# Optimization experiments

Hardware: AMD Instinct MI355X
Metric: run time of the kernel (lower is better)

The kernel has to match this reference:

```python
import jax, jax.numpy as jnp
import numpy as np

B, C = 2, 128
FMAP_HW = [(256, 256), (128, 128), (64, 64), (32, 32)]
N_ROIS = 4000
POOL = (7, 7)
N_ANCH = 300000
N_POS = 1000          # anchors with match > 0 (class 1)
N_NEG = 200000        # anchors with match == -1
SHEM_POOLSIZE = 20
N_CLASSES = 2


def setup_inputs() -> dict:
    key = jax.random.key(0)
    ks = jax.random.split(key, 10)
    inp = {}
    for l, (h, w) in enumerate(FMAP_HW):
        inp[f"fmap{l}"] = jax.random.normal(ks[l], (B, C, h, w), dtype=jnp.float32)
    # rois: normalized (y1, x1, y2, x2, batch_ix)
    ctr = jax.random.uniform(ks[4], (N_ROIS, 2))
    sz = jax.random.uniform(ks[5], (N_ROIS, 2), minval=0.02, maxval=0.5)
    lo = jnp.clip(ctr - sz / 2, 0.0, 1.0)
    hi = jnp.clip(ctr + sz / 2, 0.0, 1.0)
    bix = jax.random.randint(ks[6], (N_ROIS, 1), 0, B).astype(jnp.float32)
    inp["rois"] = jnp.concatenate([lo, hi, bix], axis=1)
    # fixed layout for static shapes: [pos | neg | neutral]
    am = np.zeros(N_ANCH, np.int32)
    am[:N_POS] = 1
    am[N_POS:N_POS + N_NEG] = -1
    inp["anchor_matches"] = jnp.asarray(am)
    inp["class_pred_logits"] = jax.random.normal(ks[7], (N_ANCH, N_CLASSES), dtype=jnp.float32)
    inp["pred_deltas"] = jax.random.normal(ks[8], (N_ANCH, 4), dtype=jnp.float32) * 0.1
    inp["target_deltas"] = jax.random.normal(ks[9], (N_ANCH, 4), dtype=jnp.float32) * 0.1
    return inp


def _roi_align_2d(fmap, boxes, batch_ix, pool):
    """Bilinear ROI align, one sample at each bin center.
    fmap: [B,C,H,W]; boxes: [N,4] in fmap pixel coords (y1,x1,y2,x2).
    Returns [N,C,ph,pw]."""
    Hc, Wc = fmap.shape[2], fmap.shape[3]
    ph, pw = pool
    y1, x1, y2, x2 = boxes[:, 0], boxes[:, 1], boxes[:, 2], boxes[:, 3]
    bh = (y2 - y1) / ph
    bw = (x2 - x1) / pw
    iy = jnp.arange(ph, dtype=jnp.float32) + 0.5
    ix = jnp.arange(pw, dtype=jnp.float32) + 0.5
    sy = jnp.clip(y1[:, None] + bh[:, None] * iy[None, :], 0.0, Hc - 1.0)  # [N,ph]
    sx = jnp.clip(x1[:, None] + bw[:, None] * ix[None, :], 0.0, Wc - 1.0)  # [N,pw]
    y0f = jnp.floor(sy)
    x0f = jnp.floor(sx)
    y0 = y0f.astype(jnp.int32)
    x0 = x0f.astype(jnp.int32)
    y1i = jnp.minimum(y0 + 1, Hc - 1)
    x1i = jnp.minimum(x0 + 1, Wc - 1)
    wy = (sy - y0f)[:, :, None, None]  # [N,ph,1,1]
    wx = (sx - x0f)[:, None, :, None]  # [N,1,pw,1]
    b = batch_ix[:, None, None]

    def gather(yy, xx):
        # yy [N,ph], xx [N,pw] -> [N,ph,pw,C]
        return fmap[b, :, yy[:, :, None], xx[:, None, :]]

    v00 = gather(y0, x0)
    v01 = gather(y0, x1i)
    v10 = gather(y1i, x0)
    v11 = gather(y1i, x1i)
    out = (v00 * (1 - wy) * (1 - wx) + v01 * (1 - wy) * wx
           + v10 * wy * (1 - wx) + v11 * wy * wx)
    return jnp.transpose(out, (0, 3, 1, 2))


def _forward(fmaps, rois, anchor_matches, class_pred_logits, pred_deltas, target_deltas):
    boxes = rois[:, :4]
    batch_ix = rois[:, 4].astype(jnp.int32)
    h = boxes[:, 2] - boxes[:, 0]
    w = boxes[:, 3] - boxes[:, 1]
    roi_level = jnp.clip(
        jnp.round(4.0 + jnp.log2(jnp.sqrt(h * w + 1e-12))).astype(jnp.int32), 0, 3)
    boxes_sg = jax.lax.stop_gradient(boxes)  # original detaches level_boxes
    pooled = jnp.zeros((N_ROIS, C, POOL[0], POOL[1]), fmaps[0].dtype)
    for lvl, f in enumerate(fmaps):
        He, We = f.shape[2], f.shape[3]
        lb = boxes_sg * jnp.array([He, We, He, We], jnp.float32)
        pl = _roi_align_2d(f, lb, batch_ix, POOL)
        mask = (roi_level == lvl).astype(pl.dtype)[:, None, None, None]
        pooled = pooled + mask * pl  # each roi hits exactly one level; order preserved

    # ---- class loss with SHEM (layout: [:N_POS] pos, [N_POS:N_POS+N_NEG] neg) ----
    pos_logits = class_pred_logits[:N_POS]
    pos_targets = anchor_matches[:N_POS].astype(jnp.int32)
    pos_logp = jax.nn.log_softmax(pos_logits, axis=1)
    pos_loss = -jnp.mean(jnp.take_along_axis(pos_logp, pos_targets[:, None], axis=1))

    neg_logits = class_pred_logits[N_POS:N_POS + N_NEG]
    neg_bg_prob = jax.nn.softmax(neg_logits, axis=1)[:, 0]
    negative_count = N_POS  # max(1, n_pos)
    pool_n = min(negative_count * SHEM_POOLSIZE, N_NEG)
    order = jnp.argsort(neg_bg_prob)          # ascending bg prob = hardest first
    pool_idx = order[:pool_n]
    perm = jax.random.permutation(jax.random.key(1), pool_n)
    neg_ix = pool_idx[perm[:negative_count]]  # stochastic draw from hard pool
    neg_loss = -jnp.mean(jax.nn.log_softmax(neg_logits[neg_ix], axis=1)[:, 0])
    class_loss = (pos_loss + neg_loss) / 2.0

    # ---- bbox smooth-L1 on positives (beta=1, mean reduction) ----
    diff = jnp.abs(pred_deltas[:N_POS] - target_deltas[:N_POS])
    sl1 = jnp.where(diff < 1.0, 0.5 * diff * diff, diff - 0.5)
    bbox_loss = jnp.mean(sl1)
    return pooled, class_loss, bbox_loss


def reference(fmap0, fmap1, fmap2, fmap3, rois, anchor_matches,
              class_pred_logits, pred_deltas, target_deltas):
    return _forward([fmap0, fmap1, fmap2, fmap3], rois, anchor_matches,
                    class_pred_logits, pred_deltas, target_deltas)
```

## Files before the change

kernel.cpp:

```cpp
#include <hip/hip_runtime.h>
#include <hip/hip_bf16.h>
#include <cstdint>

#define NROIS  4000
#define NCH    128
#define NBINS  49
#define N_POSA 1000
#define N_NEGA 200000
#define POOLN  20000
#define HBITS_A 13
#define ABINS  8192
#define PBINS  4096
#define SUBN   4096
#define NTRBLK 2720
#define NPREP  106
#define NRANKA 512
#define NRANKP 40
#define TPAD   136
#define NSC    145

#define L0OFF 0ull
#define L1OFF 16777216ull
#define L2OFF 20971520ull
#define L3OFF 22020096ull
#define TLELEMS 22282240ull

__device__ __forceinline__ uint32_t rotl32d(uint32_t v, int r) { return (v << r) | (v >> (32-r)); }

__device__ void tf2x32(uint32_t k0, uint32_t k1, uint32_t& x0, uint32_t& x1)
{
    const uint32_t ks2 = k0 ^ k1 ^ 0x1BD11BDAu;
    const int R0[4] = {13,15,26,6};
    const int R1[4] = {17,29,16,24};
    x0 += k0; x1 += k1;
#pragma unroll
    for (int r = 0; r < 4; ++r) { x0 += x1; x1 = rotl32d(x1, R0[r]); x1 ^= x0; }
    x0 += k1;  x1 += ks2 + 1u;
#pragma unroll
    for (int r = 0; r < 4; ++r) { x0 += x1; x1 = rotl32d(x1, R1[r]); x1 ^= x0; }
    x0 += ks2; x1 += k0 + 2u;
#pragma unroll
    for (int r = 0; r < 4; ++r) { x0 += x1; x1 = rotl32d(x1, R0[r]); x1 ^= x0; }
    x0 += k0;  x1 += k1 + 3u;
#pragma unroll
    for (int r = 0; r < 4; ++r) { x0 += x1; x1 = rotl32d(x1, R1[r]); x1 ^= x0; }
    x0 += k1;  x1 += ks2 + 4u;
#pragma unroll
    for (int r = 0; r < 4; ++r) { x0 += x1; x1 = rotl32d(x1, R0[r]); x1 ^= x0; }
    x0 += ks2; x1 += k0 + 5u;
}

__device__ __forceinline__ unsigned int monobits(float x) {
    unsigned int u = __float_as_uint(x);
    return (u & 0x80000000u) ? ~u : (u | 0x80000000u);
}

__device__ __forceinline__ unsigned short f2bf(float x) {
    union { __hip_bfloat16 h; unsigned short u; } c;
    c.h = __float2bfloat16(x);
    return c.u;
}

__global__ void k_zero(unsigned int* __restrict__ h, unsigned int* __restrict__ rA,
                       unsigned int* __restrict__ rP1, unsigned int* __restrict__ rP2)
{
    const int b = blockIdx.x;
    const int i = b*256 + threadIdx.x;
    if      (b <  64) h[i] = 0u;
    else if (b <  96) rA[i - 64*256] = 0u;
    else if (b < 112) rP1[i - 96*256] = 0u;
    else              rP2[i - 112*256] = 0u;
}

__global__ __launch_bounds__(256) void k_trprep(
    const float* __restrict__ f0, const float* __restrict__ f1,
    const float* __restrict__ f2, const float* __restrict__ f3,
    __hip_bfloat16* __restrict__ tl,
    unsigned long long* __restrict__ T1, unsigned long long* __restrict__ T2,
    unsigned int* __restrict__ histA,
    unsigned int* __restrict__ histP1, unsigned int* __restrict__ histP2,
    const int* __restrict__ am, const float* __restrict__ logits,
    const float* __restrict__ pd, const float* __restrict__ td,
    float* __restrict__ prt, int ntr)
{
    __shared__ __align__(16) unsigned char smraw[32768];
    const int bid = blockIdx.x;
    const int t   = threadIdx.x;

    if (bid < ntr) {
        unsigned short* s = (unsigned short*)smraw;
        const int bz = bid / 1360;
        const int r  = bid - bz*1360;
        int lvl, tile;
        if      (r < 1024) { lvl = 0; tile = r; }
        else if (r < 1280) { lvl = 1; tile = r - 1024; }
        else if (r < 1344) { lvl = 2; tile = r - 1280; }
        else               { lvl = 3; tile = r - 1344; }
        const int HW = 65536 >> (2*lvl);
        const float* in = (lvl==0) ? f0 : (lvl==1) ? f1 : (lvl==2) ? f2 : f3;
        const size_t ooff = (lvl==0) ? L0OFF : (lvl==1) ? L1OFF : (lvl==2) ? L2OFF : L3OFF;
        const int hw0 = tile * 64;
        const float4* in4 = (const float4*)(in + (size_t)bz * 128 * HW);
        const int HW4 = HW >> 2;
        const int h4b = hw0 >> 2;
#pragma unroll
        for (int k = 0; k < 8; ++k) {
            const int idx = t + k*256;
            const int c   = idx >> 4;
            const int h4  = idx & 15;
            const float4 v = in4[(size_t)c * HW4 + h4b + h4];
            const int r0 = h4 * 4;
            const int cs = c ^ ((h4 & 7) << 3);
            s[(r0+0)*TPAD + cs] = f2bf(v.x);
            s[(r0+1)*TPAD + cs] = f2bf(v.y);
            s[(r0+2)*TPAD + cs] = f2bf(v.z);
            s[(r0+3)*TPAD + cs] = f2bf(v.w);
        }
        __syncthreads();
        uint4* out4 = (uint4*)(tl + ooff + (size_t)bz * (size_t)HW * 128
                                         + (size_t)hw0 * 128);
        const int rr = t >> 4;
        const int q  = t & 15;
        const int c8 = q * 8;
#pragma unroll
        for (int m = 0; m < 4; ++m) {
            const int row = rr + m*16;
            const int sw = ((row >> 2) & 7) << 3;
            out4[row*16 + q] = *(const uint4*)&s[row*TPAD + (c8 ^ sw)];
        }
        return;
    }

    const int pbid = bid - ntr;
    if (pbid < 40) {
        unsigned int* buf = (unsigned int*)smraw;
        unsigned int* lh1 = buf;
        unsigned int* lh2 = buf + PBINS;
        for (int b = t; b < 2*PBINS; b += 256) buf[b] = 0u;
        __syncthreads();
        const int i = pbid*256 + t;
        if (i < POOLN/2) {
            uint32_t a0 = 0u, a1 = 2u; tf2x32(0u, 1u, a0, a1);
            uint32_t b0 = 1u, b1 = 3u; tf2x32(0u, 1u, b0, b1);
            uint32_t c0 = 0u, c1 = 2u; tf2x32(a0, b0, c0, c1);
            uint32_t d0 = 1u, d1 = 3u; tf2x32(a0, b0, d0, d1);
            uint32_t x0 = (uint32_t)i, x1 = (uint32_t)(POOLN/2 + i);
            tf2x32(a1, b1, x0, x1);
            T1[i]           = ((unsigned long long)x0 << 32) | (unsigned)i;
            T1[POOLN/2 + i] = ((unsigned long long)x1 << 32) | (unsigned)(POOLN/2 + i);
            atomicAdd(&lh1[x0 >> 20], 1u);
            atomicAdd(&lh1[x1 >> 20], 1u);
            uint32_t y0 = (uint32_t)i, y1 = (uint32_t)(POOLN/2 + i);
            tf2x32(c1, d1, y0, y1);
            T2[i]           = ((unsigned long long)y0 << 32) | (unsigned)i;
            T2[POOLN/2 + i] = ((unsigned long long)y1 << 32) | (unsigned)(POOLN/2 + i);
            atomicAdd(&lh2[y0 >> 20], 1u);
            atomicAdd(&lh2[y1 >> 20], 1u);
        }
        __syncthreads();
        for (int b = t; b < PBINS; b += 256) {
            unsigned int v = lh1[b]; if (v) atomicAdd(&histP1[b], v);
            v = lh2[b];              if (v) atomicAdd(&histP2[b], v);
        }
        return;
    }
    if (pbid < 104) {
        unsigned int* buf = (unsigned int*)smraw;
        for (int b = t; b < ABINS; b += 256) buf[b] = 0u;
        __syncthreads();
        for (int i = (pbid-40)*256 + t; i < N_NEGA; i += 64*256) {
            const float l0 = logits[(size_t)(N_POSA+i)*2+0];
            const float l1 = logits[(size_t)(N_POSA+i)*2+1];
            atomicAdd(&buf[monobits(l0 - l1) >> (32-HBITS_A)], 1u);
        }
        __syncthreads();
        for (int b = t; b < ABINS; b += 256) {
            const unsigned int v = buf[b];
            if (v) atomicAdd(&histA[b], v);
        }
        return;
    }
    float* red = (float*)smraw;
    float s = 0.0f;
    if (pbid == 104) {
        for (int i = t; i < N_POSA; i += 256) {
            const int tgt = am[i];
            const float l0 = logits[(size_t)i*2+0], l1 = logits[(size_t)i*2+1];
            const float m = fmaxf(l0, l1);
            const float lse = logf(expf(l0-m) + expf(l1-m));
            const float lt = (tgt == 0) ? l0 : l1;
            s += (lt - m) - lse;
        }
    } else {
        for (int i = t; i < N_POSA*4; i += 256) {
            const float d = fabsf(pd[i] - td[i]);
            s += (d < 1.0f) ? 0.5f*d*d : d - 0.5f;
        }
    }
    red[t] = s;
    __syncthreads();
    for (int off = 128; off > 0; off >>= 1) {
        if (t < off) red[t] += red[t+off];
        __syncthreads();
    }
    if (t == 0) prt[pbid - 104] = red[0];
}

__device__ void scan_one256(const unsigned int* __restrict__ hist,
                            unsigned int* __restrict__ base, int n, unsigned int* lds)
{
    const int t = threadIdx.x;
    const int chunk = n >> 8;
    unsigned int s = 0;
    for (int k = 0; k < chunk; ++k) s += hist[t*chunk + k];
    lds[t] = s;
    __syncthreads();
    for (int off = 1; off < 256; off <<= 1) {
        unsigned int v = (t >= off) ? lds[t-off] : 0u;
        __syncthreads();
        lds[t] += v;
        __syncthreads();
    }
    unsigned int run = (t == 0) ? 0u : lds[t-1];
    for (int k = 0; k < chunk; ++k) {
        base[t*chunk+k] = run;
        run += hist[t*chunk+k];
    }
    if (t == 255) base[n] = run;
    __syncthreads();
}

__device__ void do_roi(int n, const __hip_bfloat16* __restrict__ tl,
                       const float* __restrict__ rois, float* __restrict__ out,
                       unsigned char* smraw)
{
    int   (*s_a)[4] = (int(*)[4])smraw;
    float (*s_w)[4] = (float(*)[4])(smraw + 784);
    float* s_o      = (float*)(smraw + 1568);
    const int tid = threadIdx.x;

    const float ry1 = rois[n*5+0], rx1 = rois[n*5+1];
    const float ry2 = rois[n*5+2], rx2 = rois[n*5+3];
    const int   b   = (int)rois[n*5+4];
    const float h = ry2 - ry1, w = rx2 - rx1;
    const float lraw = rintf(4.0f + log2f(sqrtf(h*w + 1e-12f)));
    int lvl = (int)lraw; lvl = lvl < 0 ? 0 : (lvl > 3 ? 3 : lvl);
    const int H = 256 >> lvl;
    const size_t lbase = (lvl==0) ? L0OFF : (lvl==1) ? L1OFF : (lvl==2) ? L2OFF : L3OFF;
    const __hip_bfloat16* bp = tl + lbase + (size_t)b * (size_t)(H*H) * NCH;

    const float Hf  = (float)H;
    const float y1p = ry1*Hf, x1p = rx1*Hf, y2p = ry2*Hf, x2p = rx2*Hf;
    const float bh = (y2p - y1p) / 7.0f, bw = (x2p - x1p) / 7.0f;

    if (tid < NBINS) {
        const int py = tid / 7, px = tid % 7;
        float sy = y1p + bh*((float)py + 0.5f);
        float sx = x1p + bw*((float)px + 0.5f);
        sy = fminf(fmaxf(sy, 0.0f), Hf - 1.0f);
        sx = fminf(fmaxf(sx, 0.0f), Hf - 1.0f);
        const float y0f = floorf(sy), x0f = floorf(sx);
        const int y0 = (int)y0f, x0 = (int)x0f;
        const int y1i = min(y0+1, H-1), x1i = min(x0+1, H-1);
        const float wy = sy - y0f, wx = sx - x0f;
        s_a[tid][0] = y0 *H + x0;
        s_a[tid][1] = y0 *H + x1i;
        s_a[tid][2] = y1i*H + x0;
        s_a[tid][3] = y1i*H + x1i;
        const float omy = 1.0f - wy, omx = 1.0f - wx;
        s_w[tid][0] = omy*omx; s_w[tid][1] = omy*wx;
        s_w[tid][2] = wy *omx; s_w[tid][3] = wy *wx;
    }
    __syncthreads();

    const int c4 = tid & 31;
    const int bg = tid >> 5;
    for (int bin = bg; bin < NBINS; bin += 8) {
        float a0 = 0.f, a1 = 0.f, a2 = 0.f, a3 = 0.f;
#pragma unroll
        for (int tap = 0; tap < 4; ++tap) {
            const uint2 v = *(const uint2*)(bp + (size_t)s_a[bin][tap] * NCH + 4*c4);
            const float wgt = s_w[bin][tap];
            a0 += __uint_as_float(v.x << 16)         * wgt;
            a1 += __uint_as_float(v.x & 0xffff0000u) * wgt;
            a2 += __uint_as_float(v.y << 16)         * wgt;
            a3 += __uint_as_float(v.y & 0xffff0000u) * wgt;
        }
        s_o[(4*c4+0)*NBINS + bin] = a0;
        s_o[(4*c4+1)*NBINS + bin] = a1;
        s_o[(4*c4+2)*NBINS + bin] = a2;
        s_o[(4*c4+3)*NBINS + bin] = a3;
    }
    __syncthreads();

    float4* outn = (float4*)(out + (size_t)n * (NCH*NBINS));
    const float4* so4 = (const float4*)s_o;
    for (int t4 = tid; t4 < (NCH*NBINS)/4; t4 += 256)
        outn[t4] = so4[t4];
}

__global__ __launch_bounds__(256) void k_stage3(
    const __hip_bfloat16* __restrict__ tl, const float* __restrict__ rois,
    float* __restrict__ out, const float* __restrict__ logits,
    const unsigned long long* __restrict__ T1, const unsigned long long* __restrict__ T2,
    unsigned long long* __restrict__ A,
    unsigned long long* __restrict__ P1, unsigned long long* __restrict__ P2,
    const unsigned int* __restrict__ histA,
    const unsigned int* __restrict__ histP1, const unsigned int* __restrict__ histP2,
    unsigned int* __restrict__ baseA, unsigned int* __restrict__ baseP1,
    unsigned int* __restrict__ baseP2,
    unsigned int* __restrict__ resvA, unsigned int* __restrict__ resvP1,
    unsigned int* __restrict__ resvP2,
    unsigned int* __restrict__ sel, int rcnt)
{
    __shared__ __align__(16) unsigned char smraw[26656];
    const int bid = blockIdx.x;
    const int t   = threadIdx.x;
    if (bid < rcnt) { do_roi(bid, tl, rois, out, smraw); return; }

    const int sbid = bid - rcnt;
    if (sbid == 0) {
        unsigned int* lds = (unsigned int*)smraw;
        scan_one256(histA, baseA, ABINS, lds);
        scan_one256(histP1, baseP1, PBINS, lds);
        scan_one256(histP2, baseP2, PBINS, lds);
        const int chunk = ABINS >> 8;
        for (int k = 0; k < chunk; ++k) {
            const int bin = t*chunk + k;
            if (baseA[bin] < POOLN && baseA[bin] + histA[bin] >= POOLN)
                sel[0] = (unsigned int)bin;
        }
        return;
    }
    if (sbid <= 64) {
        const int sa = sbid - 1;
        unsigned int* lh   = (unsigned int*)smraw;
        unsigned int* temp = (unsigned int*)(smraw + 16384);
        unsigned int* svl  = (unsigned int*)(smraw + 17408);
        for (int b = t; b < ABINS/2; b += 256) lh[b] = 0u;
        unsigned int s = 0;
        for (int k = 0; k < 32; ++k) s += histA[t*32 + k];
        temp[t] = s;
        __syncthreads();
        for (int off = 1; off < 256; off <<= 1) {
            const unsigned int v = (t >= off) ? temp[t-off] : 0u;
            __syncthreads();
            temp[t] += v;
            __syncthreads();
        }
        unsigned int run = (t == 0) ? 0u : temp[t-1];
        for (int k = 0; k < 32; ++k) {
            const int b = t*32 + k;
            const unsigned int hv = histA[b];
            if (run < POOLN && run + hv >= POOLN) svl[0] = (unsigned int)b;
            run += hv;
        }
        __syncthreads();
        const unsigned int selv = svl[0];
        const int start = sa * (N_NEGA/64);
        const int end   = start + (N_NEGA/64);
        for (int i = start + t; i < end; i += 256) {
            const float l0 = logits[(size_t)(N_POSA+i)*2+0];
            const float l1 = logits[(size_t)(N_POSA+i)*2+1];
            const unsigned int bin = monobits(l0 - l1) >> (32-HBITS_A);
            if (bin <= selv) atomicAdd(&lh[bin >> 1], 1u << ((bin & 1) << 4));
        }
        __syncthreads();
        run = (t == 0) ? 0u : temp[t-1];
        for (int k = 0; k < 32; k += 2) {
            const int b0 = t*32 + k;
            const unsigned int packed = lh[b0 >> 1];
            const unsigned int c0 = packed & 0xFFFFu, c1 = packed >> 16;
            unsigned int n0 = 0u, n1 = 0u;
            if (c0) n0 = run + atomicAdd(&resvA[b0], c0);
            run += histA[b0];
            if (c1) n1 = run + atomicAdd(&resvA[b0+1], c1);
            run += histA[b0+1];
            lh[b0 >> 1] = n0 | (n1 << 16);
        }
        __syncthreads();
        for (int i = start + t; i < end; i += 256) {
            const float l0 = logits[(size_t)(N_POSA+i)*2+0];
            const float l1 = logits[(size_t)(N_POSA+i)*2+1];
            const unsigned int bits = monobits(l0 - l1);
            const unsigned int bin = bits >> (32-HBITS_A);
            if (bin <= selv) {
                const unsigned int sh  = (bin & 1) << 4;
                const unsigned int old = atomicAdd(&lh[bin >> 1], 1u << sh);
                const unsigned int pos = (old >> sh) & 0xFFFFu;
                A[pos] = ((unsigned long long)bits << 32) | (unsigned)i;
            }
        }
        return;
    }
    {
        const int sp = sbid - 65;
        unsigned short* b1   = (unsigned short*)smraw;
        unsigned short* b2   = (unsigned short*)(smraw + 8192);
        unsigned int*   temp = (unsigned int*)(smraw + 16384);
        unsigned int s = 0;
        for (int k = 0; k < 16; ++k) s += histP1[t*16 + k];
        temp[t] = s;
        __syncthreads();
        for (int off = 1; off < 256; off <<= 1) {
            const unsigned int v = (t >= off) ? temp[t-off] : 0u;
            __syncthreads(); temp[t] += v; __syncthreads();
        }
        unsigned int run = (t == 0) ? 0u : temp[t-1];
        for (int k = 0; k < 16; ++k) {
            const int b = t*16 + k;
            b1[b] = (unsigned short)run;
            run += histP1[b];
        }
        __syncthreads();
        s = 0;
        for (int k = 0; k < 16; ++k) s += histP2[t*16 + k];
        temp[t] = s;
        __syncthreads();
        for (int off = 1; off < 256; off <<= 1) {
            const unsigned int v = (t >= off) ? temp[t-off] : 0u;
            __syncthreads(); temp[t] += v; __syncthreads();
        }
        run = (t == 0) ? 0u : temp[t-1];
        for (int k = 0; k < 16; ++k) {
            const int b = t*16 + k;
            b2[b] = (unsigned short)run;
            run += histP2[b];
        }
        __syncthreads();
        const int i = sp*256 + t;
        if (i < POOLN) {
            const unsigned long long k1 = T1[i];
            const unsigned int bn1 = (unsigned)(k1 >> 52);
            const unsigned int p1 = (unsigned)b1[bn1] + atomicAdd(&resvP1[bn1], 1u);
            P1[p1] = k1;
            const unsigned long long k2 = T2[i];
            const unsigned int bn2 = (unsigned)(k2 >> 52);
            const unsigned int p2 = (unsigned)b2[bn2] + atomicAdd(&resvP2[bn2], 1u);
            P2[p2] = k2;
        }
    }
}

__global__ __launch_bounds__(256) void k_roi(
    const float* __restrict__ f0, const float* __restrict__ f1,
    const float* __restrict__ f2, const float* __restrict__ f3,
    const float* __restrict__ rois, float* __restrict__ out)
{
    __shared__ int   s_a[NBINS][4];
    __shared__ float s_w[NBINS][4];
    const int n   = blockIdx.x;
    const int tid = threadIdx.x;

    const float ry1 = rois[n*5+0], rx1 = rois[n*5+1];
    const float ry2 = rois[n*5+2], rx2 = rois[n*5+3];
    const int   b   = (int)rois[n*5+4];
    const float h = ry2 - ry1, w = rx2 - rx1;
    const float lraw = rintf(4.0f + log2f(sqrtf(h*w + 1e-12f)));
    int lvl = (int)lraw; lvl = lvl < 0 ? 0 : (lvl > 3 ? 3 : lvl);
    const int H = 256 >> lvl;
    const float* f = (lvl==0) ? f0 : (lvl==1) ? f1 : (lvl==2) ? f2 : f3;

    const float Hf  = (float)H;
    const float y1p = ry1*Hf, x1p = rx1*Hf, y2p = ry2*Hf, x2p = rx2*Hf;
    const float bh = (y2p - y1p) / 7.0f, bw = (x2p - x1p) / 7.0f;

    if (tid < NBINS) {
        const int py = tid / 7, px = tid % 7;
        float sy = y1p + bh*((float)py + 0.5f);
        float sx = x1p + bw*((float)px + 0.5f);
        sy = fminf(fmaxf(sy, 0.0f), Hf - 1.0f);
        sx = fminf(fmaxf(sx, 0.0f), Hf - 1.0f);
        const float y0f = floorf(sy), x0f = floorf(sx);
        const int y0 = (int)y0f, x0 = (int)x0f;
        const int y1i = min(y0+1, H-1), x1i = min(x0+1, H-1);
        const float wy = sy - y0f, wx = sx - x0f;
        s_a[tid][0] = y0 *H + x0;
        s_a[tid][1] = y0 *H + x1i;
        s_a[tid][2] = y1i*H + x0;
        s_a[tid][3] = y1i*H + x1i;
        const float omy = 1.0f - wy, omx = 1.0f - wx;
        s_w[tid][0] = omy*omx; s_w[tid][1] = omy*wx;
        s_w[tid][2] = wy *omx; s_w[tid][3] = wy *wx;
    }
    __syncthreads();

    const int hw = H*H;
    const float* basep = f + (size_t)b * NCH * hw;
    float* outn = out + (size_t)n * (NCH*NBINS);
    for (int t = tid; t < NCH*NBINS; t += 256) {
        const int c   = t / NBINS;
        const int bin = t - c*NBINS;
        const float* p = basep + (size_t)c * hw;
        outn[t] = p[s_a[bin][0]]*s_w[bin][0] + p[s_a[bin][1]]*s_w[bin][1]
                + p[s_a[bin][2]]*s_w[bin][2] + p[s_a[bin][3]]*s_w[bin][3];
    }
}

__global__ __launch_bounds__(1024) void k_rank(
    const unsigned long long* __restrict__ A,
    const unsigned long long* __restrict__ P1, const unsigned long long* __restrict__ P2,
    const unsigned int* __restrict__ baseA,
    const unsigned int* __restrict__ baseP1, const unsigned int* __restrict__ baseP2,
    const unsigned int* __restrict__ sel,
    unsigned int* __restrict__ As, unsigned int* __restrict__ P1s,
    unsigned int* __restrict__ P2s)
{
    __shared__ unsigned long long g[SUBN];
    __shared__ unsigned int h2[SUBN];
    __shared__ unsigned int h2b[SUBN];
    const int bid = blockIdx.x;
    const int t   = threadIdx.x;
    if (bid < NRANKA) {
        const unsigned int selv = sel[0];
        for (unsigned int bin = (unsigned)bid; bin <= selv; bin += NRANKA) {
            const int base = (int)baseA[bin];
            const int cnt  = (int)baseA[bin+1] - base;
            if (cnt <= 0) continue;
            if (cnt == 1) {
                if (t == 0) As[base] = (unsigned)(A[base] & 0xffffffffu);
                continue;
            }
            if (cnt <= SUBN) {
                for (int b = t; b < SUBN; b += 1024) h2[b] = 0u;
                __syncthreads();
                for (int k = t; k < cnt; k += 1024) {
                    const unsigned int sub = ((unsigned)(A[base+k] >> 32) >> 7) & (SUBN-1);
                    atomicAdd(&h2[sub], 1u);
                }
                __syncthreads();
                unsigned int c0 = h2[4*t+0], c1 = h2[4*t+1],
                             c2 = h2[4*t+2], c3 = h2[4*t+3];
                h2b[t] = c0 + c1 + c2 + c3;
                __syncthreads();
                for (int off = 1; off < 1024; off <<= 1) {
                    const unsigned int v = (t >= off) ? h2b[t-off] : 0u;
                    __syncthreads();
                    h2b[t] += v;
                    __syncthreads();
                }
                unsigned int run = (t == 0) ? 0u : h2b[t-1];
                __syncthreads();
                h2[4*t+0] = run; h2b[4*t+0] = run; run += c0;
                h2[4*t+1] = run; h2b[4*t+1] = run; run += c1;
                h2[4*t+2] = run; h2b[4*t+2] = run; run += c2;
                h2[4*t+3] = run; h2b[4*t+3] = run; run += c3;
                __syncthreads();
                for (int k = t; k < cnt; k += 1024) {
                    const unsigned long long key = A[base+k];
                    const unsigned int sub = ((unsigned)(key >> 32) >> 7) & (SUBN-1);
                    const unsigned int p = atomicAdd(&h2[sub], 1u);
                    g[p] = key;
                }
                __syncthreads();
                for (int p = t; p < cnt; p += 1024) {
                    const unsigned long long key = g[p];
                    const unsigned int sub = ((unsigned)(key >> 32) >> 7) & (SUBN-1);
                    const int b0 = (int)h2b[sub], e0 = (int)h2[sub];
                    int r = b0;
                    for (int q = b0; q < e0; ++q) r += (g[q] < key) ? 1 : 0;
                    As[base + r] = (unsigned)(key & 0xffffffffu);
                }
                __syncthreads();
            } else {
                for (int k = t; k < cnt; k += 1024) {
                    const unsigned long long key = A[base+k];
                    int rank = 0;
                    for (int j = 0; j < cnt; ++j) rank += (A[base+j] < key) ? 1 : 0;
                    As[base + rank] = (unsigned)(key & 0xffffffffu);
                }
            }
        }
        return;
    }
    const int gg = (bid - NRANKA)*1024 + t;
    if (gg < POOLN) {
        const unsigned long long key = P1[gg];
        const unsigned int bin = (unsigned)(key >> 52);
        const int b0 = (int)baseP1[bin], b1 = (int)baseP1[bin+1];
        int rank = 0;
        for (int j = b0; j < b1; ++j) rank += (P1[j] < key) ? 1 : 0;
        P1s[b0 + rank] = (unsigned)(key & 0xffffffffu);
    } else if (gg < 2*POOLN) {
        const int e = gg - POOLN;
        const unsigned long long key = P2[e];
        const unsigned int bin = (unsigned)(key >> 52);
        const int b0 = (int)baseP2[bin], b1 = (int)baseP2[bin+1];
        int rank = 0;
        for (int j = b0; j < b1; ++j) rank += (P2[j] < key) ? 1 : 0;
        P2s[b0 + rank] = (unsigned)(key & 0xffffffffu);
    }
}

__global__ __launch_bounds__(256) void k_final(
    const float* __restrict__ logits, const unsigned int* __restrict__ As,
    const unsigned int* __restrict__ P1s, const unsigned int* __restrict__ P2s,
    const float* __restrict__ partial, float* __restrict__ out2)
{
    __shared__ float red[256];
    const int t = threadIdx.x;
    float s = 0.0f;
    for (int j = t; j < N_POSA; j += 256) {
        const unsigned int i2 = P2s[j];
        const unsigned int r  = P1s[i2];
        const unsigned int i  = As[r];
        const float l0 = logits[(size_t)(N_POSA+i)*2+0];
        const float l1 = logits[(size_t)(N_POSA+i)*2+1];
        const float m = fmaxf(l0, l1);
        s += (l0 - m) - logf(expf(l0-m) + expf(l1-m));
    }
    red[t] = s;
    __syncthreads();
    for (int off = 128; off > 0; off >>= 1) {
        if (t < off) red[t] += red[t+off];
        __syncthreads();
    }
    if (t == 0) {
        const float neg_loss = -red[0] / (float)N_POSA;
        const float pos_loss = -partial[0] / (float)N_POSA;
        out2[0] = 0.5f * (pos_loss + neg_loss);
        out2[1] = partial[1] / (float)(N_POSA*4);
    }
}

extern "C" void kernel_launch(void* const* d_in, const int* in_sizes, int n_in,
                              void* d_out, int out_size, void* d_ws, size_t ws_size,
                              hipStream_t stream)
{
    const float* f0     = (const float*)d_in[0];
    const float* f1     = (const float*)d_in[1];
    const float* f2     = (const float*)d_in[2];
    const float* f3     = (const float*)d_in[3];
    const float* rois   = (const float*)d_in[4];
    const int*   am     = (const int*)  d_in[5];
    const float* logits = (const float*)d_in[6];
    const float* pd     = (const float*)d_in[7];
    const float* td     = (const float*)d_in[8];
    float* out = (float*)d_out;

    char* ws = (char*)d_ws;
    unsigned long long* A      = (unsigned long long*)(ws);
    unsigned long long* T1     = (unsigned long long*)(ws +  262144);
    unsigned long long* T2     = (unsigned long long*)(ws +  422144);
    unsigned long long* P1     = (unsigned long long*)(ws +  582144);
    unsigned long long* P2     = (unsigned long long*)(ws +  742144);
    unsigned int*       histA  = (unsigned int*)      (ws +  902144);
    unsigned int*       histP1 = (unsigned int*)      (ws +  934912);
    unsigned int*       histP2 = (unsigned int*)      (ws +  951296);
    unsigned int*       baseA  = (unsigned int*)      (ws +  967680);
    unsigned int*       resvA  = (unsigned int*)      (ws + 1000512);
    unsigned int*       baseP1 = (unsigned int*)      (ws + 1033344);
    unsigned int*       resvP1 = (unsigned int*)      (ws + 1049792);
    unsigned int*       baseP2 = (unsigned int*)      (ws + 1066240);
    unsigned int*       resvP2 = (unsigned int*)      (ws + 1082688);
    unsigned int*       sel    = (unsigned int*)      (ws + 1099136);
    float*              prt    = (float*)             (ws + 1099200);
    __hip_bfloat16*     tl     = (__hip_bfloat16*)    (ws + 1099264);
    unsigned int*       As     = (unsigned int*)T1;
    unsigned int*       P1s    = (unsigned int*)T2;
    unsigned int*       P2s    = (unsigned int*)((char*)T2 + 80000);
    const size_t NEED = 1099264ull + TLELEMS * 2ull;
    const bool use_cl = (ws_size >= NEED);
    const int rcnt = use_cl ? NROIS : 0;

    k_zero<<<128, 256, 0, stream>>>(histA, resvA, resvP1, resvP2);

    k_trprep<<<(use_cl ? NTRBLK : 0) + NPREP, 256, 0, stream>>>(
        f0, f1, f2, f3, tl, T1, T2, histA, histP1, histP2,
        am, logits, pd, td, prt, use_cl ? NTRBLK : 0);

    if (!use_cl)
        k_roi<<<NROIS, 256, 0, stream>>>(f0, f1, f2, f3, rois, out);

    k_stage3<<<rcnt + 144, 256, 0, stream>>>(tl, rois, out, logits,
                                             T1, T2, A, P1, P2,
                                             histA, histP1, histP2,
                                             baseA, baseP1, baseP2,
                                             resvA, resvP1, resvP2, sel, rcnt);

    k_rank<<<NRANKA + NRANKP, 1024, 0, stream>>>(A, P1, P2, baseA, baseP1, baseP2,
                                                 sel, As, P1s, P2s);

    k_final<<<1, 256, 0, stream>>>(logits, As, P1s, P2s, prt,
                                   out + (size_t)NROIS*NCH*NBINS);
}
```

Baseline: 100.4 us.

## Split ROI-align channel staging into halves with 16-byte loads for occupancy

The ROI pooling path now processes the 128 channels in two halves of 64. Each thread loads 8 bf16 channels with 16-byte loads, and only half the output tile is staged in LDS at a time. This cuts the shared buffer from about 26.6KB to 17.4KB, and launch bounds request 8 blocks per CU, to raise occupancy and reduce load instruction count. In exchange it adds an extra barrier per ROI and more registers per thread, and the smaller LDS buffer must still fit the other stage3 branches.

```diff
diff --git a/kernel.cpp b/kernel.cpp
--- a/kernel.cpp
+++ b/kernel.cpp
@@ -17,7 +17,6 @@
 #define NRANKA 512
 #define NRANKP 40
 #define TPAD   136
-#define NSC    145
 
 #define L0OFF 0ull
 #define L1OFF 16777216ull
@@ -273,33 +272,45 @@
     }
     __syncthreads();
 
-    const int c4 = tid & 31;
-    const int bg = tid >> 5;
-    for (int bin = bg; bin < NBINS; bin += 8) {
-        float a0 = 0.f, a1 = 0.f, a2 = 0.f, a3 = 0.f;
-#pragma unroll
-        for (int tap = 0; tap < 4; ++tap) {
-            const uint2 v = *(const uint2*)(bp + (size_t)s_a[bin][tap] * NCH + 4*c4);
-            const float wgt = s_w[bin][tap];
-            a0 += __uint_as_float(v.x << 16)         * wgt;
-            a1 += __uint_as_float(v.x & 0xffff0000u) * wgt;
-            a2 += __uint_as_float(v.y << 16)         * wgt;
-            a3 += __uint_as_float(v.y & 0xffff0000u) * wgt;
-        }
-        s_o[(4*c4+0)*NBINS + bin] = a0;
-        s_o[(4*c4+1)*NBINS + bin] = a1;
-        s_o[(4*c4+2)*NBINS + bin] = a2;
-        s_o[(4*c4+3)*NBINS + bin] = a3;
-    }
-    __syncthreads();
-
-    float4* outn = (float4*)(out + (size_t)n * (NCH*NBINS));
-    const float4* so4 = (const float4*)s_o;
-    for (int t4 = tid; t4 < (NCH*NBINS)/4; t4 += 256)
-        outn[t4] = so4[t4];
-}
-
-__global__ __launch_bounds__(256) void k_stage3(
+    const int c8 = tid & 7;
+    const int bg = tid >> 3;
+#pragma unroll
+    for (int half = 0; half < 2; ++half) {
+        if (half) __syncthreads();
+        for (int bin = bg; bin < NBINS; bin += 32) {
+            float a0=0.f,a1=0.f,a2=0.f,a3=0.f,a4=0.f,a5=0.f,a6=0.f,a7=0.f;
+#pragma unroll
+            for (int tap = 0; tap < 4; ++tap) {
+                const uint4 v = *(const uint4*)
+                    (bp + (size_t)s_a[bin][tap]*NCH + half*64 + 8*c8);
+                const float wgt = s_w[bin][tap];
+                a0 += __uint_as_float(v.x << 16)         * wgt;
+                a1 += __uint_as_float(v.x & 0xffff0000u) * wgt;
+                a2 += __uint_as_float(v.y << 16)         * wgt;
+                a3 += __uint_as_float(v.y & 0xffff0000u) * wgt;
+                a4 += __uint_as_float(v.z << 16)         * wgt;
+                a5 += __uint_as_float(v.z & 0xffff0000u) * wgt;
+                a6 += __uint_as_float(v.w << 16)         * wgt;
+                a7 += __uint_as_float(v.w & 0xffff0000u) * wgt;
+            }
+            s_o[(8*c8+0)*NBINS + bin] = a0;
+            s_o[(8*c8+1)*NBINS + bin] = a1;
+            s_o[(8*c8+2)*NBINS + bin] = a2;
+            s_o[(8*c8+3)*NBINS + bin] = a3;
+            s_o[(8*c8+4)*NBINS + bin] = a4;
+            s_o[(8*c8+5)*NBINS + bin] = a5;
+            s_o[(8*c8+6)*NBINS + bin] = a6;
+            s_o[(8*c8+7)*NBINS + bin] = a7;
+        }
+        __syncthreads();
+        float4* outn = (float4*)(out + (size_t)n*(NCH*NBINS) + half*64*NBINS);
+        const float4* so4 = (const float4*)s_o;
+        for (int t4 = tid; t4 < (64*NBINS)/4; t4 += 256)
+            outn[t4] = so4[t4];
+    }
+}
+
+__global__ __launch_bounds__(256, 8) void k_stage3(
     const __hip_bfloat16* __restrict__ tl, const float* __restrict__ rois,
     float* __restrict__ out, const float* __restrict__ logits,
     const unsigned long long* __restrict__ T1, const unsigned long long* __restrict__ T2,
@@ -313,7 +324,7 @@
     unsigned int* __restrict__ resvP2,
     unsigned int* __restrict__ sel, int rcnt)
 {
-    __shared__ __align__(16) unsigned char smraw[26656];
+    __shared__ __align__(16) unsigned char smraw[17440];
     const int bid = blockIdx.x;
     const int t   = threadIdx.x;
     if (bid < rcnt) { do_roi(bid, tl, rois, out, smraw); return; }
```

Result: faster. 98.13 us, median of 2 (-2.3%).
